# Kernel tuning notes

Hardware: AMD Instinct MI355X
Metric: run time of the kernel (lower is better)

The kernel has to match this reference:

```python
import jax, jax.numpy as jnp
import numpy as np

H = 256
LOG_STD_MIN, LOG_STD_MAX = -20.0, 2.0


def setup_inputs() -> dict:
    key = jax.random.key(0)
    ks = jax.random.split(key, 12)
    B, T, F, A = 256, 1000, 64, 16
    s_in = 1.0 / np.sqrt(H)
    inp = {
        "observations": jax.random.normal(ks[0], (B, T, F), jnp.float32),
        # LSTM params (PyTorch gate order: i, f, g, o)
        "W_ih": jax.random.uniform(ks[1], (4 * H, F), jnp.float32, -s_in, s_in),
        "W_hh": jax.random.uniform(ks[2], (4 * H, H), jnp.float32, -s_in, s_in),
        "b_ih": jax.random.uniform(ks[3], (4 * H,), jnp.float32, -s_in, s_in),
        "b_hh": jax.random.uniform(ks[4], (4 * H,), jnp.float32, -s_in, s_in),
        # layer2: Linear(256 -> 256)
        "W2": jax.random.uniform(ks[5], (H, H), jnp.float32, -s_in, s_in),
        "b2": jax.random.uniform(ks[6], (H,), jnp.float32, -s_in, s_in),
        # means head: Linear(256 -> A)
        "Wm": jax.random.uniform(ks[7], (A, H), jnp.float32, -s_in, s_in),
        "bm": jax.random.uniform(ks[8], (A,), jnp.float32, -s_in, s_in),
        # log_stds head: Linear(256 -> A)
        "Ws": jax.random.uniform(ks[9], (A, H), jnp.float32, -s_in, s_in),
        "bs": jax.random.uniform(ks[10], (A,), jnp.float32, -s_in, s_in),
    }
    return inp


def _lstm(observations, W_ih, W_hh, b_ih, b_hh):
    B, T, F = observations.shape
    # Precompute the input-to-gate projection for all timesteps: [T, B, 4H]
    xg = jnp.einsum("btf,gf->tbg", observations, W_ih) + (b_ih + b_hh)
    W_hh_T = W_hh.T  # [H, 4H]

    def step(carry, xg_t):
        h, c = carry  # [B, H] each
        gates = xg_t + h @ W_hh_T  # [B, 4H]
        i, f, g, o = jnp.split(gates, 4, axis=-1)
        i = jax.nn.sigmoid(i)
        f = jax.nn.sigmoid(f)
        g = jnp.tanh(g)
        o = jax.nn.sigmoid(o)
        c = f * c + i * g
        h = o * jnp.tanh(c)
        return (h, c), h

    h0 = jnp.zeros((B, H), observations.dtype)
    c0 = jnp.zeros((B, H), observations.dtype)
    _, hs = jax.lax.scan(step, (h0, c0), xg)  # hs: [T, B, H]
    return jnp.transpose(hs, (1, 0, 2))  # [B, T, H]


def reference(observations, W_ih, W_hh, b_ih, b_hh, W2, b2, Wm, bm, Ws, bs):
    x = _lstm(observations, W_ih, W_hh, b_ih, b_hh)  # [B, T, H]
    x = jax.nn.relu(jnp.einsum("bth,oh->bto", x, W2) + b2)  # [B, T, H]
    means = jnp.einsum("bth,ah->bta", x, Wm) + bm  # [B, T, A]
    log_stds = jnp.einsum("bth,ah->bta", x, Ws) + bs  # [B, T, A]
    stds = jnp.exp(jnp.clip(log_stds, LOG_STD_MIN, LOG_STD_MAX))
    return (means, stds)
```

## Files before the change

### kernel.cpp

```cpp
#include <hip/hip_runtime.h>


#define NB 256
#define NT 1000
#define NF 64
#define NH 256
#define NG 1024
#define NA 16
#define NTHREADS 512
#define CHUNK 8
#define NCHUNK (NT / CHUNK)

typedef _Float16 h2 __attribute__((ext_vector_type(2)));
typedef _Float16 h8 __attribute__((ext_vector_type(8)));
typedef float f4 __attribute__((ext_vector_type(4)));

__device__ __forceinline__ float fdot2(h2 a, h2 b, float c) {
  return __builtin_amdgcn_fdot2(a, b, c, false);
}
__device__ __forceinline__ float fexp2(float x) { return __builtin_amdgcn_exp2f(x); }
__device__ __forceinline__ float frcp(float x) { return __builtin_amdgcn_rcpf(x); }
__device__ __forceinline__ float sigmoidf_(float x) {
  return frcp(1.f + fexp2(-1.4426950408889634f * x));
}
__device__ __forceinline__ float tanhfast(float x) {
  float a = fabsf(x);
  float e = fexp2(-2.8853900817779268f * a);
  float r = (1.f - e) * frcp(1.f + e);
  return __builtin_copysignf(r, x);
}
__device__ __forceinline__ float dot8(h8 x, h8 w, float acc) {
  acc = fdot2(__builtin_shufflevector(x, x, 0, 1), __builtin_shufflevector(w, w, 0, 1), acc);
  acc = fdot2(__builtin_shufflevector(x, x, 2, 3), __builtin_shufflevector(w, w, 2, 3), acc);
  acc = fdot2(__builtin_shufflevector(x, x, 4, 5), __builtin_shufflevector(w, w, 4, 5), acc);
  acc = fdot2(__builtin_shufflevector(x, x, 6, 7), __builtin_shufflevector(w, w, 6, 7), acc);
  return acc;
}

__global__ void prep_kernel(const float* __restrict__ Wih, const float* __restrict__ Whh,
                            const float* __restrict__ bih, const float* __restrict__ bhh,
                            const float* __restrict__ W2, const float* __restrict__ Wm,
                            const float* __restrict__ Ws,
                            h2* __restrict__ whh, h2* __restrict__ wih,
                            h2* __restrict__ w2w, h2* __restrict__ wmh,
                            float* __restrict__ bg) {
  int i = blockIdx.x * 256 + threadIdx.x;
  if (i < 1024 * 128) {
    int j = i >> 7, p = i & 127;
    whh[i] = h2{(_Float16)Whh[j * 256 + 2 * p], (_Float16)Whh[j * 256 + 2 * p + 1]};
  }
  if (i < 1024 * 32) {
    int j = i >> 5, p = i & 31;
    wih[i] = h2{(_Float16)Wih[j * 64 + 2 * p], (_Float16)Wih[j * 64 + 2 * p + 1]};
  }
  if (i < 256 * 128) {
    int j = i >> 7, p = i & 127;
    w2w[i] = h2{(_Float16)W2[j * 256 + 2 * p], (_Float16)W2[j * 256 + 2 * p + 1]};
  }
  if (i < 32 * 128) {
    int j = i >> 7, p = i & 127;
    float v0, v1;
    if (j < 16) { v0 = Wm[j * 256 + 2 * p]; v1 = Wm[j * 256 + 2 * p + 1]; }
    else        { v0 = Ws[(j - 16) * 256 + 2 * p]; v1 = Ws[(j - 16) * 256 + 2 * p + 1]; }
    wmh[i] = h2{(_Float16)v0, (_Float16)v1};
  }
  if (i < 1024) bg[i] = bih[i] + bhh[i];
}

__global__ __launch_bounds__(NTHREADS, 2) void actor_kernel(
    const float* __restrict__ obs,
    const h2* __restrict__ whh, const h2* __restrict__ wih,
    const h2* __restrict__ w2w, const h2* __restrict__ wmh,
    const float* __restrict__ bg, const float* __restrict__ b2,
    const float* __restrict__ bm, const float* __restrict__ bs,
    float* __restrict__ out) {
  __shared__ __align__(16) h8 whh_l[8 * 1024];
  __shared__ __align__(16) _Float16 xg_l[CHUNK * NG];
  __shared__ __align__(16) float gbuf[NG];
  __shared__ __align__(16) h2 hbuf[NH / 2];
  __shared__ __align__(16) h2 hch[CHUNK * NH / 2];
  __shared__ __align__(16) h2 xbuf[CHUNK * NF / 2];
  __shared__ __align__(16) h2 x2b[CHUNK * NH / 2];

  const int tid = threadIdx.x;
  const int b = blockIdx.x;
  const int r0 = tid, r1 = tid + NTHREADS;

  h8 wa8[24], wb8[24];
  {
    const volatile h8* vw = (const volatile h8*)whh;
#pragma unroll
    for (int j = 0; j < 24; j++) wa8[j] = vw[r0 * 32 + 8 + j];
#pragma unroll
    for (int j = 0; j < 24; j++) wb8[j] = vw[r1 * 32 + 8 + j];
  }
  {
    const h8* whh8 = (const h8*)whh;
    for (int k = tid; k < 8 * 1024; k += NTHREADS) {
      int p4 = k >> 10, row = k & 1023;
      whh_l[p4 * 1024 + row] = whh8[row * 32 + p4];
    }
  }
  if (tid < NH / 2) hbuf[tid] = h2{(_Float16)0.f, (_Float16)0.f};
  float c_state = 0.f;
  const float biasg0 = bg[r0], biasg1 = bg[r1];
  const float b2v = b2[tid & 255];
  const int oh = tid & 31;
  const float hbv = (oh < NA) ? bm[oh] : bs[oh - NA];
  __syncthreads();

  const float* obs_b = obs + (size_t)b * NT * NF;
  float* out_means = out;
  float* out_stds = out + (size_t)NB * NT * NA;

  for (int ch = 0; ch < NCHUNK; ++ch) {
    const int t0 = ch * CHUNK;

    if (tid < 128) {
      int t = tid >> 4, fq = tid & 15;
      f4 v = *(const f4*)(obs_b + (size_t)(t0 + t) * NF + fq * 4);
      xbuf[t * 32 + fq * 2] = h2{(_Float16)v[0], (_Float16)v[1]};
      xbuf[t * 32 + fq * 2 + 1] = h2{(_Float16)v[2], (_Float16)v[3]};
    }
    __syncthreads();

#pragma unroll
    for (int rr = 0; rr < 2; ++rr) {
      const int row = rr ? r1 : r0;
      const float bias = rr ? biasg1 : biasg0;
      float acc[CHUNK];
#pragma unroll
      for (int t = 0; t < CHUNK; t++) acc[t] = bias;
      const h8* wrow = (const h8*)wih + row * 8;
#pragma unroll
      for (int jh = 0; jh < 2; jh++) {
        h8 w[4];
#pragma unroll
        for (int q = 0; q < 4; q++) w[q] = wrow[jh * 4 + q];
#pragma unroll
        for (int t = 0; t < CHUNK; t++) {
#pragma unroll
          for (int q = 0; q < 4; q++) {
            h8 xv = *(const h8*)&xbuf[t * 32 + jh * 16 + q * 4];
            acc[t] = dot8(xv, w[q], acc[t]);
          }
        }
      }
#pragma unroll
      for (int t = 0; t < CHUNK; t++) xg_l[t * NG + row] = (_Float16)acc[t];
    }
    __syncthreads();

    for (int t = 0; t < CHUNK; t++) {
      float a0a = (float)xg_l[t * NG + r0], a0b = 0.f;
      float a1a = (float)xg_l[t * NG + r1], a1b = 0.f;
#pragma unroll
      for (int p4 = 0; p4 < 8; p4++) {
        h8 hv = *(const h8*)&hbuf[p4 * 4];
        h8 w0 = whh_l[p4 * 1024 + r0];
        h8 w1 = whh_l[p4 * 1024 + r1];
        if (p4 & 1) { a0b = dot8(hv, w0, a0b); a1b = dot8(hv, w1, a1b); }
        else        { a0a = dot8(hv, w0, a0a); a1a = dot8(hv, w1, a1a); }
      }
#pragma unroll
      for (int j = 0; j < 24; j++) {
        h8 hv = *(const h8*)&hbuf[32 + 4 * j];
        if (j & 1) { a0b = dot8(hv, wa8[j], a0b); a1b = dot8(hv, wb8[j], a1b); }
        else       { a0a = dot8(hv, wa8[j], a0a); a1a = dot8(hv, wb8[j], a1a); }
      }
      gbuf[r0] = a0a + a0b;
      gbuf[r1] = a1a + a1b;
      __syncthreads();
      if (tid < NH) {
        float gi = sigmoidf_(gbuf[tid]);
        float gf = sigmoidf_(gbuf[NH + tid]);
        float gg = tanhfast(gbuf[2 * NH + tid]);
        float go = sigmoidf_(gbuf[3 * NH + tid]);
        c_state = gf * c_state + gi * gg;
        float hval = go * tanhfast(c_state);
        _Float16 hh = (_Float16)hval;
        ((_Float16*)hbuf)[tid] = hh;
        ((_Float16*)hch)[t * NH + tid] = hh;
      }
      __syncthreads();
    }

    {
      const int o = tid & 255;
      const int tb = (tid >> 8) * 4;
      float acc[4] = {b2v, b2v, b2v, b2v};
      const h8* wrow = (const h8*)w2w + o * 32;
#pragma unroll 2
      for (int c = 0; c < 8; c++) {
        h8 w[4];
#pragma unroll
        for (int q = 0; q < 4; q++) w[q] = wrow[c * 4 + q];
#pragma unroll
        for (int tt = 0; tt < 4; tt++) {
#pragma unroll
          for (int q = 0; q < 4; q++) {
            h8 xv = *(const h8*)&hch[(tb + tt) * 128 + c * 16 + q * 4];
            acc[tt] = dot8(xv, w[q], acc[tt]);
          }
        }
      }
#pragma unroll
      for (int tt = 0; tt < 4; tt++)
        ((_Float16*)x2b)[(tb + tt) * NH + o] = (_Float16)fmaxf(acc[tt], 0.f);
    }
    __syncthreads();

    if (tid < 256) {
      const int tt = tid >> 5;
      const h8* wrow = (const h8*)wmh + oh * 32;
      float acc = 0.f;
#pragma unroll 4
      for (int c = 0; c < 32; c++) {
        h8 xv = *(const h8*)&x2b[tt * 128 + c * 4];
        acc = dot8(xv, wrow[c], acc);
      }
      acc += hbv;
      const size_t idx = ((size_t)b * NT + (t0 + tt)) * NA + (oh & 15);
      if (oh < NA) {
        out_means[idx] = acc;
      } else {
        float ls = fminf(fmaxf(acc, -20.f), 2.f);
        out_stds[idx] = fexp2(1.4426950408889634f * ls);
      }
    }
  }
}

extern "C" void kernel_launch(void* const* d_in, const int* in_sizes, int n_in,
                              void* d_out, int out_size, void* d_ws, size_t ws_size,
                              hipStream_t stream) {
  const float* obs = (const float*)d_in[0];
  const float* Wih = (const float*)d_in[1];
  const float* Whh = (const float*)d_in[2];
  const float* bih = (const float*)d_in[3];
  const float* bhh = (const float*)d_in[4];
  const float* W2 = (const float*)d_in[5];
  const float* b2 = (const float*)d_in[6];
  const float* Wm = (const float*)d_in[7];
  const float* bm = (const float*)d_in[8];
  const float* Ws = (const float*)d_in[9];
  const float* bs = (const float*)d_in[10];

  char* ws = (char*)d_ws;
  h2* whh = (h2*)(ws + 0);
  h2* wih = (h2*)(ws + 524288);
  h2* w2w = (h2*)(ws + 655360);
  h2* wmh = (h2*)(ws + 786432);
  float* bg = (float*)(ws + 802816);

  prep_kernel<<<512, 256, 0, stream>>>(Wih, Whh, bih, bhh, W2, Wm, Ws,
                                       whh, wih, w2w, wmh, bg);
  actor_kernel<<<NB, NTHREADS, 0, stream>>>(obs, whh, wih, w2w, wmh, bg, b2, bm,
                                            bs, (float*)d_out);
}
```

Measured before the change: 4.475 ms.

## Split LSTM gate rows across lane quads with DPP reductions and one sync per step

Doubles the block to 1024 threads and gives each hidden unit a quad of lanes. Each lane computes one quarter of the K dimension for all four gates, and the partial sums are reduced with DPP quad permutes. This removes the shared-memory gate buffer and one barrier per timestep, and double-buffers the hidden state so each step needs only one __syncthreads. The input-projection and post-LSTM loops are reshaped to match the new thread count. It risks extra register pressure from the larger block and the tighter launch bounds.

```diff
diff --git a/kernel.cpp b/kernel.cpp
--- a/kernel.cpp
+++ b/kernel.cpp
@@ -7,7 +7,7 @@
 #define NH 256
 #define NG 1024
 #define NA 16
-#define NTHREADS 512
+#define NTHREADS 1024
 #define CHUNK 8
 #define NCHUNK (NT / CHUNK)
 
@@ -35,6 +35,11 @@
   acc = fdot2(__builtin_shufflevector(x, x, 4, 5), __builtin_shufflevector(w, w, 4, 5), acc);
   acc = fdot2(__builtin_shufflevector(x, x, 6, 7), __builtin_shufflevector(w, w, 6, 7), acc);
   return acc;
+}
+template <int CTRL>
+__device__ __forceinline__ float qperm(float x) {
+  return __int_as_float(
+      __builtin_amdgcn_update_dpp(0, __float_as_int(x), CTRL, 0xF, 0xF, true));
 }
 
 __global__ void prep_kernel(const float* __restrict__ Wih, const float* __restrict__ Whh,
@@ -67,7 +72,7 @@
   if (i < 1024) bg[i] = bih[i] + bhh[i];
 }
 
-__global__ __launch_bounds__(NTHREADS, 2) void actor_kernel(
+__global__ __launch_bounds__(NTHREADS, 4) void actor_kernel(
     const float* __restrict__ obs,
     const h2* __restrict__ whh, const h2* __restrict__ wih,
     const h2* __restrict__ w2w, const h2* __restrict__ wmh,
@@ -75,35 +80,38 @@
     const float* __restrict__ bm, const float* __restrict__ bs,
     float* __restrict__ out) {
   __shared__ __align__(16) h8 whh_l[8 * 1024];
-  __shared__ __align__(16) _Float16 xg_l[CHUNK * NG];
-  __shared__ __align__(16) float gbuf[NG];
-  __shared__ __align__(16) h2 hbuf[NH / 2];
+  __shared__ __align__(16) _Float16 xg_l[CHUNK * NTHREADS];
+  __shared__ __align__(16) h2 hbuf[2][NH / 2];
   __shared__ __align__(16) h2 hch[CHUNK * NH / 2];
   __shared__ __align__(16) h2 xbuf[CHUNK * NF / 2];
   __shared__ __align__(16) h2 x2b[CHUNK * NH / 2];
 
   const int tid = threadIdx.x;
   const int b = blockIdx.x;
-  const int r0 = tid, r1 = tid + NTHREADS;
-
-  h8 wa8[24], wb8[24];
+  const int u = tid >> 2;
+  const int k = tid & 3;
+  const int R = k * 256 + u;
+
+  h8 wreg[24];
   {
     const volatile h8* vw = (const volatile h8*)whh;
 #pragma unroll
-    for (int j = 0; j < 24; j++) wa8[j] = vw[r0 * 32 + 8 + j];
-#pragma unroll
-    for (int j = 0; j < 24; j++) wb8[j] = vw[r1 * 32 + 8 + j];
+    for (int g = 0; g < 4; g++)
+#pragma unroll
+      for (int j = 0; j < 6; j++)
+        wreg[g * 6 + j] = vw[(g * 256 + u) * 32 + k * 8 + 2 + j];
   }
   {
     const h8* whh8 = (const h8*)whh;
-    for (int k = tid; k < 8 * 1024; k += NTHREADS) {
-      int p4 = k >> 10, row = k & 1023;
-      whh_l[p4 * 1024 + row] = whh8[row * 32 + p4];
-    }
-  }
-  if (tid < NH / 2) hbuf[tid] = h2{(_Float16)0.f, (_Float16)0.f};
+#pragma unroll
+    for (int g = 0; g < 4; g++)
+#pragma unroll
+      for (int s = 0; s < 2; s++)
+        whh_l[(g * 2 + s) * 1024 + tid] = whh8[(g * 256 + u) * 32 + k * 8 + s];
+  }
+  if (tid < NH / 2) hbuf[0][tid] = h2{(_Float16)0.f, (_Float16)0.f};
   float c_state = 0.f;
-  const float biasg0 = bg[r0], biasg1 = bg[r1];
+  const float biasg = bg[R];
   const float b2v = b2[tid & 255];
   const int oh = tid & 31;
   const float hbv = (oh < NA) ? bm[oh] : bs[oh - NA];
@@ -124,89 +132,92 @@
     }
     __syncthreads();
 
-#pragma unroll
-    for (int rr = 0; rr < 2; ++rr) {
-      const int row = rr ? r1 : r0;
-      const float bias = rr ? biasg1 : biasg0;
+    {
       float acc[CHUNK];
 #pragma unroll
-      for (int t = 0; t < CHUNK; t++) acc[t] = bias;
-      const h8* wrow = (const h8*)wih + row * 8;
-#pragma unroll
-      for (int jh = 0; jh < 2; jh++) {
-        h8 w[4];
-#pragma unroll
-        for (int q = 0; q < 4; q++) w[q] = wrow[jh * 4 + q];
+      for (int t = 0; t < CHUNK; t++) acc[t] = biasg;
+      const h8* wrow = (const h8*)wih + R * 8;
+#pragma unroll
+      for (int jh = 0; jh < 4; jh++) {
+        h8 w0 = wrow[jh * 2];
+        h8 w1 = wrow[jh * 2 + 1];
 #pragma unroll
         for (int t = 0; t < CHUNK; t++) {
-#pragma unroll
-          for (int q = 0; q < 4; q++) {
-            h8 xv = *(const h8*)&xbuf[t * 32 + jh * 16 + q * 4];
-            acc[t] = dot8(xv, w[q], acc[t]);
-          }
+          h8 x0 = *(const h8*)&xbuf[t * 32 + jh * 8];
+          h8 x1 = *(const h8*)&xbuf[t * 32 + jh * 8 + 4];
+          acc[t] = dot8(x0, w0, acc[t]);
+          acc[t] = dot8(x1, w1, acc[t]);
         }
       }
 #pragma unroll
-      for (int t = 0; t < CHUNK; t++) xg_l[t * NG + row] = (_Float16)acc[t];
-    }
-    __syncthreads();
+      for (int t = 0; t < CHUNK; t++) xg_l[t * NTHREADS + tid] = (_Float16)acc[t];
+    }
 
     for (int t = 0; t < CHUNK; t++) {
-      float a0a = (float)xg_l[t * NG + r0], a0b = 0.f;
-      float a1a = (float)xg_l[t * NG + r1], a1b = 0.f;
-#pragma unroll
-      for (int p4 = 0; p4 < 8; p4++) {
-        h8 hv = *(const h8*)&hbuf[p4 * 4];
-        h8 w0 = whh_l[p4 * 1024 + r0];
-        h8 w1 = whh_l[p4 * 1024 + r1];
-        if (p4 & 1) { a0b = dot8(hv, w0, a0b); a1b = dot8(hv, w1, a1b); }
-        else        { a0a = dot8(hv, w0, a0a); a1a = dot8(hv, w1, a1a); }
-      }
-#pragma unroll
-      for (int j = 0; j < 24; j++) {
-        h8 hv = *(const h8*)&hbuf[32 + 4 * j];
-        if (j & 1) { a0b = dot8(hv, wa8[j], a0b); a1b = dot8(hv, wb8[j], a1b); }
-        else       { a0a = dot8(hv, wa8[j], a0a); a1a = dot8(hv, wb8[j], a1a); }
-      }
-      gbuf[r0] = a0a + a0b;
-      gbuf[r1] = a1a + a1b;
-      __syncthreads();
-      if (tid < NH) {
-        float gi = sigmoidf_(gbuf[tid]);
-        float gf = sigmoidf_(gbuf[NH + tid]);
-        float gg = tanhfast(gbuf[2 * NH + tid]);
-        float go = sigmoidf_(gbuf[3 * NH + tid]);
-        c_state = gf * c_state + gi * gg;
-        float hval = go * tanhfast(c_state);
+      const _Float16* hb = (const _Float16*)hbuf[t & 1] + k * 64;
+      float xgv = (float)xg_l[t * NTHREADS + tid];
+      float p0 = (k == 0) ? xgv : 0.f;
+      float p1 = (k == 1) ? xgv : 0.f;
+      float p2 = (k == 2) ? xgv : 0.f;
+      float p3 = (k == 3) ? xgv : 0.f;
+#pragma unroll
+      for (int s = 0; s < 2; s++) {
+        h8 hv = *(const h8*)(hb + s * 8);
+        p0 = dot8(hv, whh_l[(0 + s) * 1024 + tid], p0);
+        p1 = dot8(hv, whh_l[(2 + s) * 1024 + tid], p1);
+        p2 = dot8(hv, whh_l[(4 + s) * 1024 + tid], p2);
+        p3 = dot8(hv, whh_l[(6 + s) * 1024 + tid], p3);
+      }
+#pragma unroll
+      for (int j = 0; j < 6; j++) {
+        h8 hv = *(const h8*)(hb + 16 + j * 8);
+        p0 = dot8(hv, wreg[j], p0);
+        p1 = dot8(hv, wreg[6 + j], p1);
+        p2 = dot8(hv, wreg[12 + j], p2);
+        p3 = dot8(hv, wreg[18 + j], p3);
+      }
+      p0 += qperm<0xB1>(p0);
+      p1 += qperm<0xB1>(p1);
+      p2 += qperm<0xB1>(p2);
+      p3 += qperm<0xB1>(p3);
+      p0 += qperm<0x4E>(p0);
+      p1 += qperm<0x4E>(p1);
+      p2 += qperm<0x4E>(p2);
+      p3 += qperm<0x4E>(p3);
+      float gi = sigmoidf_(p0);
+      float gf = sigmoidf_(p1);
+      float gg = tanhfast(p2);
+      float go = sigmoidf_(p3);
+      c_state = gf * c_state + gi * gg;
+      float hval = go * tanhfast(c_state);
+      if (k == 0) {
         _Float16 hh = (_Float16)hval;
-        ((_Float16*)hbuf)[tid] = hh;
-        ((_Float16*)hch)[t * NH + tid] = hh;
+        ((_Float16*)hbuf[(t + 1) & 1])[u] = hh;
+        ((_Float16*)hch)[t * NH + u] = hh;
       }
       __syncthreads();
     }
 
     {
       const int o = tid & 255;
-      const int tb = (tid >> 8) * 4;
-      float acc[4] = {b2v, b2v, b2v, b2v};
+      const int tb = (tid >> 8) * 2;
+      float acc0 = b2v, acc1 = b2v;
       const h8* wrow = (const h8*)w2w + o * 32;
 #pragma unroll 2
-      for (int c = 0; c < 8; c++) {
-        h8 w[4];
-#pragma unroll
-        for (int q = 0; q < 4; q++) w[q] = wrow[c * 4 + q];
-#pragma unroll
-        for (int tt = 0; tt < 4; tt++) {
-#pragma unroll
-          for (int q = 0; q < 4; q++) {
-            h8 xv = *(const h8*)&hch[(tb + tt) * 128 + c * 16 + q * 4];
-            acc[tt] = dot8(xv, w[q], acc[tt]);
-          }
-        }
-      }
-#pragma unroll
-      for (int tt = 0; tt < 4; tt++)
-        ((_Float16*)x2b)[(tb + tt) * NH + o] = (_Float16)fmaxf(acc[tt], 0.f);
+      for (int c = 0; c < 16; c++) {
+        h8 w0 = wrow[c * 2];
+        h8 w1 = wrow[c * 2 + 1];
+        h8 x0 = *(const h8*)&hch[tb * 128 + c * 8];
+        h8 x0b = *(const h8*)&hch[tb * 128 + c * 8 + 4];
+        h8 x1 = *(const h8*)&hch[(tb + 1) * 128 + c * 8];
+        h8 x1b = *(const h8*)&hch[(tb + 1) * 128 + c * 8 + 4];
+        acc0 = dot8(x0, w0, acc0);
+        acc0 = dot8(x0b, w1, acc0);
+        acc1 = dot8(x1, w0, acc1);
+        acc1 = dot8(x1b, w1, acc1);
+      }
+      ((_Float16*)x2b)[tb * NH + o] = (_Float16)fmaxf(acc0, 0.f);
+      ((_Float16*)x2b)[(tb + 1) * NH + o] = (_Float16)fmaxf(acc1, 0.f);
     }
     __syncthreads();
 
@@ -214,7 +225,7 @@
       const int tt = tid >> 5;
       const h8* wrow = (const h8*)wmh + oh * 32;
       float acc = 0.f;
-#pragma unroll 4
+#pragma unroll 2
       for (int c = 0; c < 32; c++) {
         h8 xv = *(const h8*)&x2b[tt * 128 + c * 4];
         acc = dot8(xv, wrow[c], acc);
```

Result: slower. 7.553 ms (+68.8%).

## Split LSTM recurrence by hidden unit with DPP reduction and double-buffered h

Applied to the files above, without the earlier changes.

Reassigns the recurrent matvec so each pair of threads owns one hidden unit's four gates, each thread covering half of the hidden input, and combines the halves with a DPP lane swap instead of a shared gate buffer. This removes one of the two block barriers per timestep and lets all threads compute gate activations, with h double-buffered and padded to limit bank conflicts. The gate projections are stored interleaved per unit so each thread reads its four input-gate values with a single load. Register weight usage stays at 48 h8 per thread while the LDS weight layout is reorganised per thread.

```diff
diff --git a/kernel.cpp b/kernel.cpp
--- a/kernel.cpp
+++ b/kernel.cpp
@@ -10,8 +10,10 @@
 #define NTHREADS 512
 #define CHUNK 8
 #define NCHUNK (NT / CHUNK)
+#define HHALF 68
 
 typedef _Float16 h2 __attribute__((ext_vector_type(2)));
+typedef _Float16 h4 __attribute__((ext_vector_type(4)));
 typedef _Float16 h8 __attribute__((ext_vector_type(8)));
 typedef float f4 __attribute__((ext_vector_type(4)));
 
@@ -35,6 +37,11 @@
   acc = fdot2(__builtin_shufflevector(x, x, 4, 5), __builtin_shufflevector(w, w, 4, 5), acc);
   acc = fdot2(__builtin_shufflevector(x, x, 6, 7), __builtin_shufflevector(w, w, 6, 7), acc);
   return acc;
+}
+template <int CTRL>
+__device__ __forceinline__ float qperm(float x) {
+  return __int_as_float(
+      __builtin_amdgcn_update_dpp(0, __float_as_int(x), CTRL, 0xF, 0xF, true));
 }
 
 __global__ void prep_kernel(const float* __restrict__ Wih, const float* __restrict__ Whh,
@@ -74,36 +81,38 @@
     const float* __restrict__ bg, const float* __restrict__ b2,
     const float* __restrict__ bm, const float* __restrict__ bs,
     float* __restrict__ out) {
-  __shared__ __align__(16) h8 whh_l[8 * 1024];
+  __shared__ __align__(16) h8 whh_l[16 * NTHREADS];
   __shared__ __align__(16) _Float16 xg_l[CHUNK * NG];
-  __shared__ __align__(16) float gbuf[NG];
-  __shared__ __align__(16) h2 hbuf[NH / 2];
+  __shared__ __align__(16) h2 hbuf[2][2 * HHALF];
   __shared__ __align__(16) h2 hch[CHUNK * NH / 2];
   __shared__ __align__(16) h2 xbuf[CHUNK * NF / 2];
   __shared__ __align__(16) h2 x2b[CHUNK * NH / 2];
 
   const int tid = threadIdx.x;
   const int b = blockIdx.x;
-  const int r0 = tid, r1 = tid + NTHREADS;
-
-  h8 wa8[24], wb8[24];
+  const int q = tid >> 1;
+  const int jhalf = tid & 1;
+
+  h8 wreg[48];
   {
     const volatile h8* vw = (const volatile h8*)whh;
 #pragma unroll
-    for (int j = 0; j < 24; j++) wa8[j] = vw[r0 * 32 + 8 + j];
-#pragma unroll
-    for (int j = 0; j < 24; j++) wb8[j] = vw[r1 * 32 + 8 + j];
+    for (int g = 0; g < 4; g++)
+#pragma unroll
+      for (int jj = 0; jj < 12; jj++)
+        wreg[g * 12 + jj] = vw[(g * 256 + q) * 32 + jhalf * 16 + 4 + jj];
   }
   {
     const h8* whh8 = (const h8*)whh;
-    for (int k = tid; k < 8 * 1024; k += NTHREADS) {
-      int p4 = k >> 10, row = k & 1023;
-      whh_l[p4 * 1024 + row] = whh8[row * 32 + p4];
-    }
-  }
-  if (tid < NH / 2) hbuf[tid] = h2{(_Float16)0.f, (_Float16)0.f};
+#pragma unroll
+    for (int g = 0; g < 4; g++)
+#pragma unroll
+      for (int s = 0; s < 4; s++)
+        whh_l[(g * 4 + s) * NTHREADS + tid] = whh8[(g * 256 + q) * 32 + jhalf * 16 + s];
+  }
+  if (tid < 2 * HHALF) hbuf[0][tid] = h2{(_Float16)0.f, (_Float16)0.f};
   float c_state = 0.f;
-  const float biasg0 = bg[r0], biasg1 = bg[r1];
+  const float bg0 = bg[tid], bg1 = bg[tid + 512];
   const float b2v = b2[tid & 255];
   const int oh = tid & 31;
   const float hbv = (oh < NA) ? bm[oh] : bs[oh - NA];
@@ -126,8 +135,8 @@
 
 #pragma unroll
     for (int rr = 0; rr < 2; ++rr) {
-      const int row = rr ? r1 : r0;
-      const float bias = rr ? biasg1 : biasg0;
+      const int row = tid + rr * 512;
+      const float bias = rr ? bg1 : bg0;
       float acc[CHUNK];
 #pragma unroll
       for (int t = 0; t < CHUNK; t++) acc[t] = bias;
@@ -136,51 +145,57 @@
       for (int jh = 0; jh < 2; jh++) {
         h8 w[4];
 #pragma unroll
-        for (int q = 0; q < 4; q++) w[q] = wrow[jh * 4 + q];
+        for (int qq = 0; qq < 4; qq++) w[qq] = wrow[jh * 4 + qq];
 #pragma unroll
         for (int t = 0; t < CHUNK; t++) {
 #pragma unroll
-          for (int q = 0; q < 4; q++) {
-            h8 xv = *(const h8*)&xbuf[t * 32 + jh * 16 + q * 4];
-            acc[t] = dot8(xv, w[q], acc[t]);
+          for (int qq = 0; qq < 4; qq++) {
+            h8 xv = *(const h8*)&xbuf[t * 32 + jh * 16 + qq * 4];
+            acc[t] = dot8(xv, w[qq], acc[t]);
           }
         }
       }
-#pragma unroll
-      for (int t = 0; t < CHUNK; t++) xg_l[t * NG + row] = (_Float16)acc[t];
+      const int g = row >> 8, uu = row & 255;
+#pragma unroll
+      for (int t = 0; t < CHUNK; t++)
+        xg_l[(t * 256 + uu) * 4 + g] = (_Float16)acc[t];
     }
     __syncthreads();
 
     for (int t = 0; t < CHUNK; t++) {
-      float a0a = (float)xg_l[t * NG + r0], a0b = 0.f;
-      float a1a = (float)xg_l[t * NG + r1], a1b = 0.f;
-#pragma unroll
-      for (int p4 = 0; p4 < 8; p4++) {
-        h8 hv = *(const h8*)&hbuf[p4 * 4];
-        h8 w0 = whh_l[p4 * 1024 + r0];
-        h8 w1 = whh_l[p4 * 1024 + r1];
-        if (p4 & 1) { a0b = dot8(hv, w0, a0b); a1b = dot8(hv, w1, a1b); }
-        else        { a0a = dot8(hv, w0, a0a); a1a = dot8(hv, w1, a1a); }
-      }
-#pragma unroll
-      for (int j = 0; j < 24; j++) {
-        h8 hv = *(const h8*)&hbuf[32 + 4 * j];
-        if (j & 1) { a0b = dot8(hv, wa8[j], a0b); a1b = dot8(hv, wb8[j], a1b); }
-        else       { a0a = dot8(hv, wa8[j], a0a); a1a = dot8(hv, wb8[j], a1a); }
-      }
-      gbuf[r0] = a0a + a0b;
-      gbuf[r1] = a1a + a1b;
-      __syncthreads();
-      if (tid < NH) {
-        float gi = sigmoidf_(gbuf[tid]);
-        float gf = sigmoidf_(gbuf[NH + tid]);
-        float gg = tanhfast(gbuf[2 * NH + tid]);
-        float go = sigmoidf_(gbuf[3 * NH + tid]);
-        c_state = gf * c_state + gi * gg;
-        float hval = go * tanhfast(c_state);
+      const _Float16* hb = (const _Float16*)&hbuf[t & 1][jhalf * HHALF];
+      h4 xg4 = *(const h4*)&xg_l[(t * 256 + q) * 4];
+      float p0 = 0.f, p1 = 0.f, p2 = 0.f, p3 = 0.f;
+#pragma unroll
+      for (int s = 0; s < 4; s++) {
+        h8 hv = *(const h8*)(hb + s * 8);
+        p0 = dot8(hv, whh_l[(0 * 4 + s) * NTHREADS + tid], p0);
+        p1 = dot8(hv, whh_l[(1 * 4 + s) * NTHREADS + tid], p1);
+        p2 = dot8(hv, whh_l[(2 * 4 + s) * NTHREADS + tid], p2);
+        p3 = dot8(hv, whh_l[(3 * 4 + s) * NTHREADS + tid], p3);
+      }
+#pragma unroll
+      for (int jj = 0; jj < 12; jj++) {
+        h8 hv = *(const h8*)(hb + 32 + jj * 8);
+        p0 = dot8(hv, wreg[jj], p0);
+        p1 = dot8(hv, wreg[12 + jj], p1);
+        p2 = dot8(hv, wreg[24 + jj], p2);
+        p3 = dot8(hv, wreg[36 + jj], p3);
+      }
+      p0 += qperm<0xB1>(p0);
+      p1 += qperm<0xB1>(p1);
+      p2 += qperm<0xB1>(p2);
+      p3 += qperm<0xB1>(p3);
+      float gi = sigmoidf_(p0 + (float)xg4[0]);
+      float gf = sigmoidf_(p1 + (float)xg4[1]);
+      float gg = tanhfast(p2 + (float)xg4[2]);
+      float go = sigmoidf_(p3 + (float)xg4[3]);
+      c_state = gf * c_state + gi * gg;
+      float hval = go * tanhfast(c_state);
+      if (jhalf == 0) {
         _Float16 hh = (_Float16)hval;
-        ((_Float16*)hbuf)[tid] = hh;
-        ((_Float16*)hch)[t * NH + tid] = hh;
+        ((_Float16*)&hbuf[(t + 1) & 1][(q >> 7) * HHALF])[q & 127] = hh;
+        ((_Float16*)hch)[t * NH + q] = hh;
       }
       __syncthreads();
     }
@@ -194,13 +209,13 @@
       for (int c = 0; c < 8; c++) {
         h8 w[4];
 #pragma unroll
-        for (int q = 0; q < 4; q++) w[q] = wrow[c * 4 + q];
+        for (int qq = 0; qq < 4; qq++) w[qq] = wrow[c * 4 + qq];
 #pragma unroll
         for (int tt = 0; tt < 4; tt++) {
 #pragma unroll
-          for (int q = 0; q < 4; q++) {
-            h8 xv = *(const h8*)&hch[(tb + tt) * 128 + c * 16 + q * 4];
-            acc[tt] = dot8(xv, w[q], acc[tt]);
+          for (int qq = 0; qq < 4; qq++) {
+            h8 xv = *(const h8*)&hch[(tb + tt) * 128 + c * 16 + qq * 4];
+            acc[tt] = dot8(xv, w[qq], acc[tt]);
           }
         }
       }
```

After: 4.554 ms. About the same (+1.8%).
